# Kernel tuning notes

Hardware: AMD Instinct MI355X
Metric: run time of the kernel (lower is better)

The kernel has to match this reference:

```python
import jax, jax.numpy as jnp
import numpy as np
import math

CH = 512
HEADS = 8
GROUPS = 32
EPS = 1e-5


def group_norm(x, w, b):
    # x: [B, C, T]
    B, C, T = x.shape
    xg = x.reshape(B, GROUPS, C // GROUPS, T)
    mu = xg.mean(axis=(2, 3), keepdims=True)
    var = xg.var(axis=(2, 3), keepdims=True)
    xg = (xg - mu) * jax.lax.rsqrt(var + EPS)
    return xg.reshape(B, C, T) * w[None, :, None] + b[None, :, None]


def conv1x1(x, w, b):
    # x: [B, C, T], w: [O, C, 1]
    return jnp.einsum('oc,bct->bot', w[:, :, 0], x) + b[None, :, None]


def conv3_same(x, w, b):
    y = jax.lax.conv_general_dilated(x, w, window_strides=(1,), padding='SAME',
                                     dimension_numbers=('NCH', 'OIH', 'NCH'))
    return y + b[None, :, None]


def setup_inputs() -> dict:
    key = jax.random.key(0)
    ks = jax.random.split(key, 12)
    B, Ti, Ts = 2, 4096, 1024
    inp = {
        'image': jax.random.normal(ks[0], (B, Ti, CH), jnp.float32),
        'st': jax.random.normal(ks[1], (B, Ts, CH), jnp.float32),
        'xn_w': jnp.ones((CH,), jnp.float32),
        'xn_b': jnp.zeros((CH,), jnp.float32),
        'jn_w': jnp.ones((CH,), jnp.float32),
        'jn_b': jnp.zeros((CH,), jnp.float32),
        'xqkv_w': jax.random.normal(ks[2], (3 * CH, CH, 1), jnp.float32) * (1.0 / math.sqrt(CH)),
        'xqkv_b': jnp.zeros((3 * CH,), jnp.float32),
        'jqkv_w': jax.random.normal(ks[3], (3 * CH, CH, 1), jnp.float32) * (1.0 / math.sqrt(CH)),
        'jqkv_b': jnp.zeros((3 * CH,), jnp.float32),
        # NOTE: original zero-inits proj; we use small random weights so the
        # attention path contributes to the output (same math).
        'proj_w': jax.random.normal(ks[4], (CH, CH, 3), jnp.float32) * (0.02 / math.sqrt(3 * CH)),
        'proj_b': jnp.zeros((CH,), jnp.float32),
    }
    return inp


def reference(image, st, xn_w, xn_b, jn_w, jn_b, xqkv_w, xqkv_b, jqkv_w, jqkv_b, proj_w, proj_b):
    # image: [B, Ti, C]  st: [B, Ts, C]
    x = image.transpose(0, 2, 1)           # [B, C, Ti]
    jc = st.transpose(0, 2, 1)              # [B, C, Ts]

    x_qkv = conv1x1(group_norm(x, xn_w, xn_b), xqkv_w, xqkv_b)    # [B, 3C, Ti]
    jc_qkv = conv1x1(group_norm(jc, jn_w, jn_b), jqkv_w, jqkv_b)  # [B, 3C, Ts]

    B, _, Ti = x_qkv.shape
    ch = CH // HEADS
    scale = 1.0 / math.sqrt(math.sqrt(ch))

    img_q = x_qkv[:, :CH].reshape(B, HEADS, ch, Ti)
    st_k = jc_qkv[:, CH:2 * CH].reshape(B, HEADS, ch, -1)
    st_v = jc_qkv[:, 2 * CH:].reshape(B, HEADS, ch, -1)

    # cross-attention: image queries attend to st keys/values
    w = jnp.einsum('bhct,bhcs->bhts', img_q * scale, st_k * scale)  # [B,H,Ti,Ts]
    w = jax.nn.softmax(w.astype(jnp.float32), axis=-1).astype(w.dtype)
    attn = jnp.einsum('bhts,bhcs->bhct', w, st_v).reshape(B, CH, Ti)

    x_h = conv3_same(attn, proj_w, proj_b)
    return x + x_h  # [B, C, Ti]
```

## Files before the change

### kernel.cpp

```cpp
#include <hip/hip_runtime.h>
#include <math.h>

static constexpr int CH = 512;
static constexpr int GROUPS = 32;
static constexpr int HC = 64;
static constexpr float EPS = 1e-5f;
static constexpr int TI = 4096;
static constexpr int TS = 1024;

typedef __bf16 bf16x8 __attribute__((ext_vector_type(8)));
typedef float f32x4 __attribute__((ext_vector_type(4)));

__global__ __launch_bounds__(256) void k_gn_stats(const float* __restrict__ X, int T,
                                                  float* __restrict__ stats) {
  int b = blockIdx.x >> 5;
  int g = blockIdx.x & 31;
  int tid = threadIdx.x;
  const float* base = X + ((size_t)b * T) * CH + g * 16;
  double s1 = 0.0, s2 = 0.0;
  for (int t = tid; t < T; t += 256) {
    const float4* p = (const float4*)(base + (size_t)t * CH);
#pragma unroll
    for (int q = 0; q < 4; ++q) {
      float4 v = p[q];
      s1 += (double)v.x + (double)v.y + (double)v.z + (double)v.w;
      s2 += (double)v.x * v.x + (double)v.y * v.y + (double)v.z * v.z + (double)v.w * v.w;
    }
  }
  __shared__ double r1[256];
  __shared__ double r2[256];
  r1[tid] = s1;
  r2[tid] = s2;
  __syncthreads();
  for (int s = 128; s > 0; s >>= 1) {
    if (tid < s) { r1[tid] += r1[tid + s]; r2[tid] += r2[tid + s]; }
    __syncthreads();
  }
  if (tid == 0) {
    double N = (double)16 * T;
    double mu = r1[0] / N;
    double var = r2[0] / N - mu * mu;
    float rs = (float)(1.0 / sqrt(var + (double)EPS));
    stats[(b * GROUPS + g) * 2 + 0] = (float)mu;
    stats[(b * GROUPS + g) * 2 + 1] = rs;
  }
}

__global__ __launch_bounds__(256) void k_gn_apply(const float* __restrict__ X,
                                                  const float* __restrict__ stats,
                                                  const float* __restrict__ nw,
                                                  const float* __restrict__ nb,
                                                  __bf16* __restrict__ Xp, int T) {
  size_t idx = ((size_t)blockIdx.x * 256 + threadIdx.x) * 8;
  int b = (int)(idx / ((size_t)T * 512));
  size_t rem = idx - (size_t)b * T * 512;
  int t = (int)(rem >> 9);
  int c = (int)(rem & 511);
  int g = c >> 4;
  float mu = stats[(b * GROUPS + g) * 2 + 0];
  float rs = stats[(b * GROUPS + g) * 2 + 1];
  float4 v0 = *(const float4*)(X + idx);
  float4 v1 = *(const float4*)(X + idx + 4);
  float4 w0 = *(const float4*)(nw + c);
  float4 w1 = *(const float4*)(nw + c + 4);
  float4 q0 = *(const float4*)(nb + c);
  float4 q1 = *(const float4*)(nb + c + 4);
  float xv[8] = {v0.x, v0.y, v0.z, v0.w, v1.x, v1.y, v1.z, v1.w};
  float wv[8] = {w0.x, w0.y, w0.z, w0.w, w1.x, w1.y, w1.z, w1.w};
  float qv[8] = {q0.x, q0.y, q0.z, q0.w, q1.x, q1.y, q1.z, q1.w};
  bf16x8 r;
#pragma unroll
  for (int i = 0; i < 8; ++i) {
    float a = rs * wv[i];
    r[i] = (__bf16)fmaf(xv[i], a, qv[i] - mu * a);
  }
  size_t off = ((((size_t)b * (T >> 4) + (t >> 4)) * 16 + (c >> 5)) * 64 +
                ((c >> 3) & 3) * 16 + (t & 15)) * 8;
  *(bf16x8*)(Xp + off) = r;
}

__global__ __launch_bounds__(256) void k_wpack(const float* __restrict__ W,
                                               __bf16* __restrict__ Wp) {
  int idx = blockIdx.x * 256 + threadIdx.x;
  int lane = idx & 63;
  int l = lane & 15, g = lane >> 4;
  int cb = (idx >> 6) & 15;
  int ob = idx >> 10;
  const float* src = W + (size_t)(ob * 16 + l) * 512 + cb * 32 + g * 8;
  float4 v0 = *(const float4*)src;
  float4 v1 = *(const float4*)(src + 4);
  float xv[8] = {v0.x, v0.y, v0.z, v0.w, v1.x, v1.y, v1.z, v1.w};
  bf16x8 r;
#pragma unroll
  for (int i = 0; i < 8; ++i) r[i] = (__bf16)xv[i];
  *(bf16x8*)(Wp + (size_t)idx * 8) = r;
}

__global__ __launch_bounds__(256) void k_wpack3(const float* __restrict__ W,
                                                __bf16* __restrict__ W3p) {
  int idx = blockIdx.x * 256 + threadIdx.x;
  int lane = idx & 63;
  int l = lane & 15, g = lane >> 4;
  int ob = (idx >> 6) & 31;
  int q = idx >> 11;
  int tap = q % 3;
  int cb = q / 3;
  int o = ob * 16 + l;
  int c = cb * 32 + g * 8;
  bf16x8 r;
#pragma unroll
  for (int j = 0; j < 8; ++j) r[j] = (__bf16)W[((size_t)o * 512 + c + j) * 3 + tap];
  *(bf16x8*)(W3p + (size_t)idx * 8) = r;
}

__global__ __launch_bounds__(256) void k_qkv_mfma(const __bf16* __restrict__ Xp,
                                                  const __bf16* __restrict__ Wp,
                                                  const float* __restrict__ bias,
                                                  __bf16* __restrict__ outQK,
                                                  __bf16* __restrict__ outVp,
                                                  int T) {
  int b = blockIdx.z;
  int o0 = blockIdx.y * 64;
  int tid = threadIdx.x;
  int w = tid >> 6;
  int lane = tid & 63;
  int l = lane & 15;
  int g = lane >> 4;
  int t0 = blockIdx.x * 128 + w * 32;
  int Tb = T >> 4;

  f32x4 acc[2][4] = {};
  const __bf16* Xb = Xp + (size_t)b * T * 512;

  auto load_c = [&](int cb, bf16x8 (&af)[2], bf16x8 (&wf)[4]) {
#pragma unroll
    for (int m = 0; m < 2; ++m)
      af[m] = *(const bf16x8*)(Xb + ((((size_t)(t0 >> 4) + m) * 16 + cb) * 64 + lane) * 8);
#pragma unroll
    for (int n = 0; n < 4; ++n)
      wf[n] = *(const bf16x8*)(Wp + ((((size_t)(o0 >> 4) + n) * 16 + cb) * 64 + lane) * 8);
  };
  auto mm = [&](const bf16x8 (&af)[2], const bf16x8 (&wf)[4]) {
#pragma unroll
    for (int m = 0; m < 2; ++m)
#pragma unroll
      for (int n = 0; n < 4; ++n)
        acc[m][n] = __builtin_amdgcn_mfma_f32_16x16x32_bf16(af[m], wf[n], acc[m][n], 0, 0, 0);
  };

  bf16x8 afA[2], wfA[4], afB[2], wfB[4];
  load_c(0, afA, wfA);
#pragma unroll
  for (int cb = 0; cb < 16; cb += 2) {
    load_c(cb + 1, afB, wfB);
    mm(afA, wfA);
    if (cb + 2 < 16) load_c(cb + 2, afA, wfA);
    mm(afB, wfB);
  }

  if (outVp == nullptr) {
#pragma unroll
    for (int m = 0; m < 2; ++m) {
#pragma unroll
      for (int n = 0; n < 4; ++n) {
        int oo = o0 + 16 * n + l;
        float bo = bias[oo];
        int cb = oo >> 5, gp = (oo >> 3) & 3, j = oo & 7;
#pragma unroll
        for (int rr = 0; rr < 4; ++rr) {
          size_t off = ((((size_t)b * Tb + (t0 >> 4) + m) * 16 + cb) * 64 +
                        gp * 16 + 4 * g + rr) * 8 + j;
          outQK[off] = (__bf16)((acc[m][n][rr] + bo) * 0.125f);
        }
      }
    }
  } else if (o0 < 512) {
#pragma unroll
    for (int m = 0; m < 2; ++m) {
#pragma unroll
      for (int n = 0; n < 4; ++n) {
        int oo = o0 + 16 * n + l;
        float bo = bias[oo];
        int cb = oo >> 5, gp = (oo >> 3) & 3, j = oo & 7;
#pragma unroll
        for (int rr = 0; rr < 4; ++rr) {
          size_t off = ((((size_t)b * Tb + (t0 >> 4) + m) * 16 + cb) * 64 +
                        gp * 16 + 4 * g + rr) * 8 + j;
          outQK[off] = (__bf16)(acc[m][n][rr] + bo);
        }
      }
    }
  } else {
#pragma unroll
    for (int m = 0; m < 2; ++m) {
#pragma unroll
      for (int n = 0; n < 4; ++n) {
        int cb16 = ((o0 - 512) >> 4) + n;
        float bo = bias[o0 + 16 * n + l];
#pragma unroll
        for (int rr = 0; rr < 4; ++rr) {
          int sl = 16 * m + 4 * g + rr;
          size_t off = ((((size_t)b * 32 + cb16) * 32 + (t0 >> 5)) * 64 +
                        (sl >> 3) * 16 + l) * 8 + (sl & 7);
          outVp[off] = (__bf16)(acc[m][n][rr] + bo);
        }
      }
    }
  }
}

__global__ __launch_bounds__(128, 4) void k_attn_mfma(const __bf16* __restrict__ Qp,
                                                      const __bf16* __restrict__ Kp,
                                                      const __bf16* __restrict__ Vp,
                                                      __bf16* __restrict__ outA) {
  int b = blockIdx.z;
  int h = blockIdx.y;
  int tid = threadIdx.x;
  int w = tid >> 6;
  int lane = tid & 63;
  int l = lane & 15;
  int g = lane >> 4;
  int t0 = blockIdx.x * 32;

  __shared__ __align__(16) __bf16 Plds[2][32][72];
  __shared__ float Ored[64][32];
  __shared__ float Lred[64][8];

  bf16x8 qf[2][2];
#pragma unroll
  for (int m = 0; m < 2; ++m)
#pragma unroll
    for (int ks = 0; ks < 2; ++ks)
      qf[m][ks] = *(const bf16x8*)(Qp + ((((size_t)b * 256 + (t0 >> 4) + m) * 16 +
                                          2 * h + ks) * 64 + lane) * 8);

  f32x4 o_acc[2][4] = {};
  float rs_acc[2][4] = {};

  int s_base = w * 512;
#pragma unroll 1
  for (int s0 = s_base; s0 < s_base + 512; s0 += 64) {
    bf16x8 kf[4][2];
#pragma unroll
    for (int n = 0; n < 4; ++n)
#pragma unroll
      for (int ks = 0; ks < 2; ++ks)
        kf[n][ks] = *(const bf16x8*)(Kp + ((((size_t)b * 64 + (s0 >> 4) + n) * 16 +
                                            2 * h + ks) * 64 + lane) * 8);
    bf16x8 vf[4][2];
#pragma unroll
    for (int n = 0; n < 4; ++n)
#pragma unroll
      for (int ks = 0; ks < 2; ++ks)
        vf[n][ks] = *(const bf16x8*)(Vp + ((((size_t)b * 32 + h * 4 + n) * 32 +
                                            (s0 >> 5) + ks) * 64 + lane) * 8);
    f32x4 s_acc[2][4];
#pragma unroll
    for (int m = 0; m < 2; ++m)
#pragma unroll
      for (int n = 0; n < 4; ++n) {
        f32x4 z = {0.f, 0.f, 0.f, 0.f};
        z = __builtin_amdgcn_mfma_f32_16x16x32_bf16(qf[m][0], kf[n][0], z, 0, 0, 0);
        s_acc[m][n] = __builtin_amdgcn_mfma_f32_16x16x32_bf16(qf[m][1], kf[n][1], z, 0, 0, 0);
      }
#pragma unroll
    for (int m = 0; m < 2; ++m)
#pragma unroll
      for (int n = 0; n < 4; ++n)
#pragma unroll
        for (int r = 0; r < 4; ++r) {
          float p = __expf(s_acc[m][n][r]);
          rs_acc[m][r] += p;
          Plds[w][16 * m + 4 * g + r][16 * n + l] = (__bf16)p;
        }
    bf16x8 pa[2][2];
#pragma unroll
    for (int m = 0; m < 2; ++m)
#pragma unroll
      for (int ks = 0; ks < 2; ++ks)
        pa[m][ks] = *(const bf16x8*)&Plds[w][16 * m + l][32 * ks + 8 * g];
#pragma unroll
    for (int m = 0; m < 2; ++m)
#pragma unroll
      for (int n = 0; n < 4; ++n) {
        o_acc[m][n] = __builtin_amdgcn_mfma_f32_16x16x32_bf16(pa[m][0], vf[n][0], o_acc[m][n], 0, 0, 0);
        o_acc[m][n] = __builtin_amdgcn_mfma_f32_16x16x32_bf16(pa[m][1], vf[n][1], o_acc[m][n], 0, 0, 0);
      }
  }

  if (w == 1) {
#pragma unroll
    for (int m = 0; m < 2; ++m)
#pragma unroll
      for (int n = 0; n < 4; ++n)
#pragma unroll
        for (int r = 0; r < 4; ++r) Ored[lane][m * 16 + n * 4 + r] = o_acc[m][n][r];
#pragma unroll
    for (int m = 0; m < 2; ++m)
#pragma unroll
      for (int r = 0; r < 4; ++r) Lred[lane][m * 4 + r] = rs_acc[m][r];
  }
  __syncthreads();
  if (w == 0) {
#pragma unroll
    for (int m = 0; m < 2; ++m)
#pragma unroll
      for (int n = 0; n < 4; ++n)
#pragma unroll
        for (int r = 0; r < 4; ++r) o_acc[m][n][r] += Ored[lane][m * 16 + n * 4 + r];
    float inv[2][4];
#pragma unroll
    for (int m = 0; m < 2; ++m)
#pragma unroll
      for (int r = 0; r < 4; ++r) {
        float v = rs_acc[m][r] + Lred[lane][m * 4 + r];
#pragma unroll
        for (int mm = 1; mm < 16; mm <<= 1) v += __shfl_xor(v, mm, 64);
        inv[m][r] = 1.f / v;
      }
#pragma unroll
    for (int m = 0; m < 2; ++m)
#pragma unroll
      for (int n = 0; n < 4; ++n)
#pragma unroll
        for (int r = 0; r < 4; ++r)
          Plds[0][16 * m + 4 * g + r][16 * n + l] = (__bf16)(o_acc[m][n][r] * inv[m][r]);
    int row = lane & 31, half = lane >> 5;
#pragma unroll
    for (int k = 0; k < 4; ++k) {
      bf16x8 v = *(const bf16x8*)&Plds[0][row][half * 32 + k * 8];
      *(bf16x8*)(outA + ((size_t)b * TI + t0 + row) * 512 + h * 64 + half * 32 + k * 8) = v;
    }
  }
}

__global__ __launch_bounds__(256) void k_conv3_mfma(const __bf16* __restrict__ A,
                                                    const __bf16* __restrict__ W3p,
                                                    const float* __restrict__ bias,
                                                    const float* __restrict__ image,
                                                    float* __restrict__ out) {
  int b = blockIdx.z;
  int o0 = blockIdx.y * 64;
  int ob0 = o0 >> 4;
  int tid = threadIdx.x;
  int w = tid >> 6;
  int lane = tid & 63;
  int l = lane & 15;
  int g = lane >> 4;
  int t0 = blockIdx.x * 128;
  int t0w = t0 + w * 32;

  __shared__ __align__(16) __bf16 Alds[2][130 * 32];
  __shared__ __align__(16) __bf16 Wlds[2][12 * 512];

  const __bf16* Ab = A + (size_t)b * TI * 512;

  auto stage = [&](int cb, int buf) {
#pragma unroll
    for (int pass = 0; pass < 3; ++pass) {
      int gi = tid + pass * 256;
      if (gi < 520) {
        int r = gi >> 2, gg = gi & 3;
        int t = t0 - 1 + r;
        bf16x8 v = {};
        if (t >= 0 && t < TI) v = *(const bf16x8*)(Ab + (size_t)t * 512 + cb * 32 + gg * 8);
        *(bf16x8*)&Alds[buf][r * 32 + ((gg ^ (r & 3)) << 3)] = v;
      }
    }
#pragma unroll
    for (int ch = w; ch < 12; ch += 4) {
      bf16x8 v = *(const bf16x8*)(W3p + ((((size_t)cb * 3 + (ch >> 2)) * 32 + ob0 +
                                          (ch & 3)) * 64 + lane) * 8);
      *(bf16x8*)&Wlds[buf][ch * 512 + lane * 8] = v;
    }
  };

  f32x4 acc[2][4] = {};

  stage(0, 0);
  __syncthreads();
#pragma unroll 1
  for (int cs = 0; cs < 16; ++cs) {
    int cur = cs & 1;
    if (cs < 15) stage(cs + 1, cur ^ 1);
    bf16x8 af[3][2], wf[3][4];
#pragma unroll
    for (int tap = 0; tap < 3; ++tap) {
#pragma unroll
      for (int m = 0; m < 2; ++m) {
        int r = w * 32 + 16 * m + l + tap;
        af[tap][m] = *(const bf16x8*)&Alds[cur][r * 32 + ((g ^ (r & 3)) << 3)];
      }
#pragma unroll
      for (int n = 0; n < 4; ++n)
        wf[tap][n] = *(const bf16x8*)&Wlds[cur][(tap * 4 + n) * 512 + lane * 8];
    }
#pragma unroll
    for (int tap = 0; tap < 3; ++tap)
#pragma unroll
      for (int m = 0; m < 2; ++m)
#pragma unroll
        for (int n = 0; n < 4; ++n)
          acc[m][n] =
              __builtin_amdgcn_mfma_f32_16x16x32_bf16(af[tap][m], wf[tap][n], acc[m][n], 0, 0, 0);
    __syncthreads();
  }

#pragma unroll
  for (int m = 0; m < 2; ++m) {
    int tb = t0w + 16 * m + 4 * g;
#pragma unroll
    for (int n = 0; n < 4; ++n) {
      int o = o0 + 16 * n + l;
      float bo = bias[o];
      f32x4 r;
#pragma unroll
      for (int rr = 0; rr < 4; ++rr)
        r[rr] = acc[m][n][rr] + bo + image[((size_t)b * TI + tb + rr) * CH + o];
      *(f32x4*)(out + ((size_t)b * CH + o) * TI + tb) = r;
    }
  }
}

extern "C" void kernel_launch(void* const* d_in, const int* in_sizes, int n_in,
                              void* d_out, int out_size, void* d_ws, size_t ws_size,
                              hipStream_t stream) {
  const float* image = (const float*)d_in[0];
  const float* st = (const float*)d_in[1];
  const float* xn_w = (const float*)d_in[2];
  const float* xn_b = (const float*)d_in[3];
  const float* jn_w = (const float*)d_in[4];
  const float* jn_b = (const float*)d_in[5];
  const float* xqkv_w = (const float*)d_in[6];
  const float* xqkv_b = (const float*)d_in[7];
  const float* jqkv_w = (const float*)d_in[8];
  const float* jqkv_b = (const float*)d_in[9];
  const float* proj_w = (const float*)d_in[10];
  const float* proj_b = (const float*)d_in[11];
  float* out = (float*)d_out;
  float* ws = (float*)d_ws;

  float* stats_x = ws;
  float* stats_j = ws + 128;
  __bf16* Xnp = (__bf16*)(ws + 256);
  __bf16* abuf = Xnp;
  __bf16* stnp = Xnp + (size_t)2 * TI * CH;
  __bf16* wqb = stnp + (size_t)2 * TS * CH;
  __bf16* wkvb = wqb + (size_t)CH * CH;
  __bf16* wb3 = wkvb + (size_t)2 * CH * CH;
  __bf16* Qp = wb3 + (size_t)3 * CH * CH;
  __bf16* Kp = Qp + (size_t)2 * TI * CH;
  __bf16* Vp = Kp + (size_t)2 * TS * CH;

  k_gn_stats<<<dim3(64), dim3(256), 0, stream>>>(image, TI, stats_x);
  k_gn_stats<<<dim3(64), dim3(256), 0, stream>>>(st, TS, stats_j);

  k_gn_apply<<<dim3(2 * TI * 512 / 2048), dim3(256), 0, stream>>>(image, stats_x, xn_w, xn_b, Xnp, TI);
  k_gn_apply<<<dim3(2 * TS * 512 / 2048), dim3(256), 0, stream>>>(st, stats_j, jn_w, jn_b, stnp, TS);

  k_wpack<<<dim3(128), dim3(256), 0, stream>>>(xqkv_w, wqb);
  k_wpack<<<dim3(256), dim3(256), 0, stream>>>(jqkv_w + (size_t)CH * CH, wkvb);
  k_wpack3<<<dim3(384), dim3(256), 0, stream>>>(proj_w, wb3);

  k_qkv_mfma<<<dim3(TI / 128, CH / 64, 2), dim3(256), 0, stream>>>(
      Xnp, wqb, xqkv_b, Qp, nullptr, TI);
  k_qkv_mfma<<<dim3(TS / 128, 1024 / 64, 2), dim3(256), 0, stream>>>(
      stnp, wkvb, jqkv_b + CH, Kp, Vp, TS);

  k_attn_mfma<<<dim3(TI / 32, 8, 2), dim3(128), 0, stream>>>(Qp, Kp, Vp, abuf);

  k_conv3_mfma<<<dim3(TI / 128, CH / 64, 2), dim3(256), 0, stream>>>(
      abuf, wb3, proj_b, image, out);
}
```

Baseline: 134.3 us.

## Transpose MFMA operands and stage epilogues through swizzled LDS for vector stores

Swaps the MFMA operand order in the QKV projection and attention kernels, so each lane's accumulator registers hold consecutive output channels or keys. Epilogues then stage bf16x4 chunks through XOR-swizzled shared memory and write bf16x8 vectors to global memory, instead of scattering scalar bf16 stores. In attention, row sums now reduce with two shuffles instead of four, and the P tile is written as vectors with a bank-conflict-avoiding swizzle. This adds 16KB of LDS per QKV block, which may lower occupancy.

```diff
diff --git a/kernel.cpp b/kernel.cpp
--- a/kernel.cpp
+++ b/kernel.cpp
@@ -9,6 +9,7 @@
 static constexpr int TS = 1024;
 
 typedef __bf16 bf16x8 __attribute__((ext_vector_type(8)));
+typedef __bf16 bf16x4 __attribute__((ext_vector_type(4)));
 typedef float f32x4 __attribute__((ext_vector_type(4)));
 
 __global__ __launch_bounds__(256) void k_gn_stats(const float* __restrict__ X, int T,
@@ -128,6 +129,9 @@
   int g = lane >> 4;
   int t0 = blockIdx.x * 128 + w * 32;
   int Tb = T >> 4;
+  bool vmode = (outVp != nullptr) && (o0 >= 512);
+
+  __shared__ __align__(16) __bf16 Elds[4][2048];
 
   f32x4 acc[2][4] = {};
   const __bf16* Xb = Xp + (size_t)b * T * 512;
@@ -140,73 +144,72 @@
     for (int n = 0; n < 4; ++n)
       wf[n] = *(const bf16x8*)(Wp + ((((size_t)(o0 >> 4) + n) * 16 + cb) * 64 + lane) * 8);
   };
-  auto mm = [&](const bf16x8 (&af)[2], const bf16x8 (&wf)[4]) {
+
+  bf16x8 afA[2], wfA[4], afB[2], wfB[4];
+#define QKV_LOOP(MMEXPR)                                                        \
+  {                                                                             \
+    load_c(0, afA, wfA);                                                        \
+    _Pragma("unroll") for (int cb = 0; cb < 16; cb += 2) {                      \
+      load_c(cb + 1, afB, wfB);                                                 \
+      _Pragma("unroll") for (int m = 0; m < 2; ++m)                             \
+          _Pragma("unroll") for (int n = 0; n < 4; ++n) {                       \
+        bf16x8 af = afA[m], wf = wfA[n];                                        \
+        acc[m][n] = MMEXPR;                                                     \
+      }                                                                         \
+      if (cb + 2 < 16) load_c(cb + 2, afA, wfA);                                \
+      _Pragma("unroll") for (int m = 0; m < 2; ++m)                             \
+          _Pragma("unroll") for (int n = 0; n < 4; ++n) {                       \
+        bf16x8 af = afB[m], wf = wfB[n];                                        \
+        acc[m][n] = MMEXPR;                                                     \
+      }                                                                         \
+    }                                                                           \
+  }
+
+  if (!vmode) {
+    QKV_LOOP(__builtin_amdgcn_mfma_f32_16x16x32_bf16(wf, af, acc[m][n], 0, 0, 0))
+    float sc = (outVp == nullptr) ? 0.125f : 1.0f;
+    int swz = (l & 7) << 1;
+    __bf16(*Eq)[64] = reinterpret_cast<__bf16(*)[64]>(&Elds[w][0]);
 #pragma unroll
     for (int m = 0; m < 2; ++m)
 #pragma unroll
-      for (int n = 0; n < 4; ++n)
-        acc[m][n] = __builtin_amdgcn_mfma_f32_16x16x32_bf16(af[m], wf[n], acc[m][n], 0, 0, 0);
-  };
-
-  bf16x8 afA[2], wfA[4], afB[2], wfB[4];
-  load_c(0, afA, wfA);
-#pragma unroll
-  for (int cb = 0; cb < 16; cb += 2) {
-    load_c(cb + 1, afB, wfB);
-    mm(afA, wfA);
-    if (cb + 2 < 16) load_c(cb + 2, afA, wfA);
-    mm(afB, wfB);
-  }
-
-  if (outVp == nullptr) {
-#pragma unroll
-    for (int m = 0; m < 2; ++m) {
-#pragma unroll
       for (int n = 0; n < 4; ++n) {
-        int oo = o0 + 16 * n + l;
-        float bo = bias[oo];
-        int cb = oo >> 5, gp = (oo >> 3) & 3, j = oo & 7;
-#pragma unroll
-        for (int rr = 0; rr < 4; ++rr) {
-          size_t off = ((((size_t)b * Tb + (t0 >> 4) + m) * 16 + cb) * 64 +
-                        gp * 16 + 4 * g + rr) * 8 + j;
-          outQK[off] = (__bf16)((acc[m][n][rr] + bo) * 0.125f);
-        }
-      }
-    }
-  } else if (o0 < 512) {
-#pragma unroll
-    for (int m = 0; m < 2; ++m) {
+        f32x4 bv = *(const f32x4*)(bias + o0 + 16 * n + 4 * g);
+        bf16x4 pv;
+#pragma unroll
+        for (int r = 0; r < 4; ++r) pv[r] = (__bf16)((acc[m][n][r] + bv[r]) * sc);
+        *(bf16x4*)&Eq[m * 16 + l][((4 * n + g) ^ swz) * 4] = pv;
+      }
+#pragma unroll
+    for (int m = 0; m < 2; ++m)
+#pragma unroll
+      for (int cbi = 0; cbi < 2; ++cbi) {
+        bf16x8 v = *(const bf16x8*)&Eq[m * 16 + l][((8 * cbi + 2 * g) ^ swz) * 4];
+        *(bf16x8*)(outQK +
+                   ((((size_t)b * Tb + (t0 >> 4) + m) * 16 + (o0 >> 5) + cbi) * 64 + lane) * 8) = v;
+      }
+  } else {
+    QKV_LOOP(__builtin_amdgcn_mfma_f32_16x16x32_bf16(af, wf, acc[m][n], 0, 0, 0))
+    int swzv = l & 6;
+    __bf16(*Ev)[32] = reinterpret_cast<__bf16(*)[32]>(&Elds[w][0]);
+#pragma unroll
+    for (int m = 0; m < 2; ++m)
 #pragma unroll
       for (int n = 0; n < 4; ++n) {
-        int oo = o0 + 16 * n + l;
-        float bo = bias[oo];
-        int cb = oo >> 5, gp = (oo >> 3) & 3, j = oo & 7;
-#pragma unroll
-        for (int rr = 0; rr < 4; ++rr) {
-          size_t off = ((((size_t)b * Tb + (t0 >> 4) + m) * 16 + cb) * 64 +
-                        gp * 16 + 4 * g + rr) * 8 + j;
-          outQK[off] = (__bf16)(acc[m][n][rr] + bo);
-        }
-      }
-    }
-  } else {
-#pragma unroll
-    for (int m = 0; m < 2; ++m) {
-#pragma unroll
-      for (int n = 0; n < 4; ++n) {
-        int cb16 = ((o0 - 512) >> 4) + n;
         float bo = bias[o0 + 16 * n + l];
-#pragma unroll
-        for (int rr = 0; rr < 4; ++rr) {
-          int sl = 16 * m + 4 * g + rr;
-          size_t off = ((((size_t)b * 32 + cb16) * 32 + (t0 >> 5)) * 64 +
-                        (sl >> 3) * 16 + l) * 8 + (sl & 7);
-          outVp[off] = (__bf16)(acc[m][n][rr] + bo);
-        }
-      }
-    }
-  }
+        bf16x4 pv;
+#pragma unroll
+        for (int r = 0; r < 4; ++r) pv[r] = (__bf16)(acc[m][n][r] + bo);
+        *(bf16x4*)&Ev[16 * n + l][((4 * m + g) ^ swzv) * 4] = pv;
+      }
+#pragma unroll
+    for (int n = 0; n < 4; ++n) {
+      bf16x8 v = *(const bf16x8*)&Ev[16 * n + l][((2 * g) ^ swzv) * 4];
+      int cb16 = ((o0 - 512) >> 4) + n;
+      *(bf16x8*)(outVp + ((((size_t)b * 32 + cb16) * 32 + (t0 >> 5)) * 64 + lane) * 8) = v;
+    }
+  }
+#undef QKV_LOOP
 }
 
 __global__ __launch_bounds__(128, 4) void k_attn_mfma(const __bf16* __restrict__ Qp,
@@ -221,10 +224,11 @@
   int l = lane & 15;
   int g = lane >> 4;
   int t0 = blockIdx.x * 32;
-
-  __shared__ __align__(16) __bf16 Plds[2][32][72];
+  int swz = (l & 7) << 1;
+
+  __shared__ __align__(16) __bf16 Pt[2][2][16][64];
   __shared__ float Ored[64][32];
-  __shared__ float Lred[64][8];
+  __shared__ float Lred[64][2];
 
   bf16x8 qf[2][2];
 #pragma unroll
@@ -235,7 +239,7 @@
                                           2 * h + ks) * 64 + lane) * 8);
 
   f32x4 o_acc[2][4] = {};
-  float rs_acc[2][4] = {};
+  float rs_acc[2] = {};
 
   int s_base = w * 512;
 #pragma unroll 1
@@ -254,82 +258,75 @@
       for (int ks = 0; ks < 2; ++ks)
         vf[n][ks] = *(const bf16x8*)(Vp + ((((size_t)b * 32 + h * 4 + n) * 32 +
                                             (s0 >> 5) + ks) * 64 + lane) * 8);
-    f32x4 s_acc[2][4];
-#pragma unroll
-    for (int m = 0; m < 2; ++m)
+    f32x4 sT[4][2];
+#pragma unroll
+    for (int sb = 0; sb < 4; ++sb)
+#pragma unroll
+      for (int tb = 0; tb < 2; ++tb) {
+        f32x4 z = {0.f, 0.f, 0.f, 0.f};
+        z = __builtin_amdgcn_mfma_f32_16x16x32_bf16(kf[sb][0], qf[tb][0], z, 0, 0, 0);
+        sT[sb][tb] = __builtin_amdgcn_mfma_f32_16x16x32_bf16(kf[sb][1], qf[tb][1], z, 0, 0, 0);
+      }
+#pragma unroll
+    for (int tb = 0; tb < 2; ++tb)
+#pragma unroll
+      for (int sb = 0; sb < 4; ++sb) {
+        float p0 = __expf(sT[sb][tb][0]);
+        float p1 = __expf(sT[sb][tb][1]);
+        float p2 = __expf(sT[sb][tb][2]);
+        float p3 = __expf(sT[sb][tb][3]);
+        rs_acc[tb] += (p0 + p1) + (p2 + p3);
+        bf16x4 pv;
+        pv[0] = (__bf16)p0;
+        pv[1] = (__bf16)p1;
+        pv[2] = (__bf16)p2;
+        pv[3] = (__bf16)p3;
+        *(bf16x4*)&Pt[w][tb][l][((4 * sb + g) ^ swz) * 4] = pv;
+      }
+    bf16x8 pa[2][2];
+#pragma unroll
+    for (int tb = 0; tb < 2; ++tb)
+#pragma unroll
+      for (int ks = 0; ks < 2; ++ks)
+        pa[tb][ks] = *(const bf16x8*)&Pt[w][tb][l][((8 * ks + 2 * g) ^ swz) * 4];
+#pragma unroll
+    for (int tb = 0; tb < 2; ++tb)
 #pragma unroll
       for (int n = 0; n < 4; ++n) {
-        f32x4 z = {0.f, 0.f, 0.f, 0.f};
-        z = __builtin_amdgcn_mfma_f32_16x16x32_bf16(qf[m][0], kf[n][0], z, 0, 0, 0);
-        s_acc[m][n] = __builtin_amdgcn_mfma_f32_16x16x32_bf16(qf[m][1], kf[n][1], z, 0, 0, 0);
-      }
-#pragma unroll
-    for (int m = 0; m < 2; ++m)
+        o_acc[tb][n] = __builtin_amdgcn_mfma_f32_16x16x32_bf16(vf[n][0], pa[tb][0], o_acc[tb][n], 0, 0, 0);
+        o_acc[tb][n] = __builtin_amdgcn_mfma_f32_16x16x32_bf16(vf[n][1], pa[tb][1], o_acc[tb][n], 0, 0, 0);
+      }
+  }
+
+  if (w == 1) {
+#pragma unroll
+    for (int tb = 0; tb < 2; ++tb) {
 #pragma unroll
       for (int n = 0; n < 4; ++n)
 #pragma unroll
-        for (int r = 0; r < 4; ++r) {
-          float p = __expf(s_acc[m][n][r]);
-          rs_acc[m][r] += p;
-          Plds[w][16 * m + 4 * g + r][16 * n + l] = (__bf16)p;
-        }
-    bf16x8 pa[2][2];
-#pragma unroll
-    for (int m = 0; m < 2; ++m)
-#pragma unroll
-      for (int ks = 0; ks < 2; ++ks)
-        pa[m][ks] = *(const bf16x8*)&Plds[w][16 * m + l][32 * ks + 8 * g];
-#pragma unroll
-    for (int m = 0; m < 2; ++m)
-#pragma unroll
-      for (int n = 0; n < 4; ++n) {
-        o_acc[m][n] = __builtin_amdgcn_mfma_f32_16x16x32_bf16(pa[m][0], vf[n][0], o_acc[m][n], 0, 0, 0);
-        o_acc[m][n] = __builtin_amdgcn_mfma_f32_16x16x32_bf16(pa[m][1], vf[n][1], o_acc[m][n], 0, 0, 0);
-      }
-  }
-
-  if (w == 1) {
-#pragma unroll
-    for (int m = 0; m < 2; ++m)
-#pragma unroll
-      for (int n = 0; n < 4; ++n)
-#pragma unroll
-        for (int r = 0; r < 4; ++r) Ored[lane][m * 16 + n * 4 + r] = o_acc[m][n][r];
-#pragma unroll
-    for (int m = 0; m < 2; ++m)
-#pragma unroll
-      for (int r = 0; r < 4; ++r) Lred[lane][m * 4 + r] = rs_acc[m][r];
+        for (int r = 0; r < 4; ++r) Ored[lane][tb * 16 + n * 4 + r] = o_acc[tb][n][r];
+      Lred[lane][tb] = rs_acc[tb];
+    }
   }
   __syncthreads();
   if (w == 0) {
 #pragma unroll
-    for (int m = 0; m < 2; ++m)
+    for (int tb = 0; tb < 2; ++tb) {
 #pragma unroll
       for (int n = 0; n < 4; ++n)
 #pragma unroll
-        for (int r = 0; r < 4; ++r) o_acc[m][n][r] += Ored[lane][m * 16 + n * 4 + r];
-    float inv[2][4];
-#pragma unroll
-    for (int m = 0; m < 2; ++m)
-#pragma unroll
-      for (int r = 0; r < 4; ++r) {
-        float v = rs_acc[m][r] + Lred[lane][m * 4 + r];
-#pragma unroll
-        for (int mm = 1; mm < 16; mm <<= 1) v += __shfl_xor(v, mm, 64);
-        inv[m][r] = 1.f / v;
-      }
-#pragma unroll
-    for (int m = 0; m < 2; ++m)
-#pragma unroll
-      for (int n = 0; n < 4; ++n)
-#pragma unroll
-        for (int r = 0; r < 4; ++r)
-          Plds[0][16 * m + 4 * g + r][16 * n + l] = (__bf16)(o_acc[m][n][r] * inv[m][r]);
-    int row = lane & 31, half = lane >> 5;
-#pragma unroll
-    for (int k = 0; k < 4; ++k) {
-      bf16x8 v = *(const bf16x8*)&Plds[0][row][half * 32 + k * 8];
-      *(bf16x8*)(outA + ((size_t)b * TI + t0 + row) * 512 + h * 64 + half * 32 + k * 8) = v;
+        for (int r = 0; r < 4; ++r) o_acc[tb][n][r] += Ored[lane][tb * 16 + n * 4 + r];
+      float v = rs_acc[tb] + Lred[lane][tb];
+      v += __shfl_xor(v, 16, 64);
+      v += __shfl_xor(v, 32, 64);
+      float inv = 1.f / v;
+#pragma unroll
+      for (int n = 0; n < 4; ++n) {
+        bf16x4 ov;
+#pragma unroll
+        for (int r = 0; r < 4; ++r) ov[r] = (__bf16)(o_acc[tb][n][r] * inv);
+        *(bf16x4*)(outA + ((size_t)b * TI + t0 + 16 * tb + l) * 512 + h * 64 + 16 * n + 4 * g) = ov;
+      }
     }
   }
 }
```

New measurement: 123.7 us. 7.9% less time.
